# Kernel tuning notes

Hardware: AMD Instinct MI355X
Metric: run time of the kernel (lower is better)

Reference implementation:

```python
import jax, jax.numpy as jnp
import numpy as np

B, S, H, A = 16, 2048, 1024, 8


def setup_inputs() -> dict:
    key = jax.random.key(0)
    k1, k2, k3, k4 = jax.random.split(key, 4)
    token_embeddings = jax.random.normal(k1, (B, S, H), dtype=jnp.float32)
    aspect_embedding = jax.random.normal(k2, (B, A, H), dtype=jnp.float32)
    # Linear(2H -> H): stored as [2H, H] so we can use x @ W (same math as torch W^T)
    W = jax.random.normal(k3, (2 * H, H), dtype=jnp.float32) * (1.0 / np.sqrt(2 * H))
    b = jnp.zeros((H,), dtype=jnp.float32)
    v = jax.random.uniform(k4, (H,), dtype=jnp.float32)  # torch.rand init
    return {"token_embeddings": token_embeddings, "aspect_embedding": aspect_embedding,
            "W": W, "b": b, "v": v}


def reference(token_embeddings, aspect_embedding, W, b, v):
    # mean-pool aspect tokens -> [B, 1, H], broadcast over seq
    asp = jnp.mean(aspect_embedding, axis=1, keepdims=True)
    asp = jnp.broadcast_to(asp, token_embeddings.shape)          # [B, S, H]
    combined = jnp.concatenate([token_embeddings, asp], axis=2)   # [B, S, 2H]
    energy = jnp.tanh(combined @ W + b)                           # [B, S, H]
    scores = jnp.einsum('bsh,h->bs', energy, v)                   # [B, S]
    weights = jax.nn.softmax(scores, axis=1)                      # [B, S]
    # token * weights + token  ==  token * (1 + weights)
    return token_embeddings * (1.0 + weights[:, :, None])
```

## Files before the change

kernel.cpp:

```cpp
#include <hip/hip_runtime.h>
#include <hip/hip_bf16.h>
#include <stdint.h>


#define SEQ 2048
#define H 1024
#define MTOT 32768
#define BK 32

typedef __bf16 bf16x8 __attribute__((ext_vector_type(8)));
typedef float  f32x4  __attribute__((ext_vector_type(4)));

__device__ __forceinline__ void async16(const void* g, void* l) {
  __builtin_amdgcn_global_load_lds(
      (const __attribute__((address_space(1))) unsigned*)g,
      (__attribute__((address_space(3))) unsigned*)l, 16, 0, 0);
}

__device__ __forceinline__ unsigned f2bfraw(float f) {
  unsigned x = __float_as_uint(f);
  return (x + 0x7fffu + ((x >> 16) & 1u)) >> 16;
}
__device__ __forceinline__ float fast_tanh(float x) {
  x = fminf(fmaxf(x, -40.0f), 40.0f);
  float e = __expf(2.0f * x);
  return 1.0f - 2.0f / (e + 1.0f);
}

__global__ __launch_bounds__(256) void convert_tok(
    const float* __restrict__ in, unsigned short* __restrict__ ob) {
  const size_t i = ((size_t)blockIdx.x * 256 + threadIdx.x) * 8;
  const f32x4 a = *reinterpret_cast<const f32x4*>(in + i);
  const f32x4 b = *reinterpret_cast<const f32x4*>(in + i + 4);
  uint4 r;
  r.x = f2bfraw(a[0]) | (f2bfraw(a[1]) << 16);
  r.y = f2bfraw(a[2]) | (f2bfraw(a[3]) << 16);
  r.z = f2bfraw(b[0]) | (f2bfraw(b[1]) << 16);
  r.w = f2bfraw(b[2]) | (f2bfraw(b[3]) << 16);
  *reinterpret_cast<uint4*>(ob + i) = r;
}

__global__ __launch_bounds__(256) void transpose_w(
    const float* __restrict__ W, unsigned short* __restrict__ WT) {
  __shared__ float tile[32][33];
  const int x = threadIdx.x;
  const int y = threadIdx.y;
  const int n0 = blockIdx.x * 32, k0 = blockIdx.y * 32;
#pragma unroll
  for (int i = 0; i < 4; ++i)
    tile[y + 8 * i][x] = W[(size_t)(k0 + y + 8 * i) * H + n0 + x];
  __syncthreads();
#pragma unroll
  for (int i = 0; i < 4; ++i)
    WT[(size_t)(n0 + y + 8 * i) * H + k0 + x] = (unsigned short)f2bfraw(tile[x][y + 8 * i]);
}

__global__ __launch_bounds__(256) void aspect_c(
    const float* __restrict__ asp,
    const float* __restrict__ W,
    const float* __restrict__ bias,
    float* __restrict__ cpart) {
  const int b = blockIdx.x, nc = blockIdx.y, kc = blockIdx.z;
  const int t = threadIdx.x;
  const int lane = t & 63, w = t >> 6;
  __shared__ float am[256];
  __shared__ f32x4 red[4][64];
  {
    const int k = kc * 256 + t;
    float s = 0.f;
#pragma unroll
    for (int a = 0; a < 8; ++a) s += asp[(size_t)(b * 8 + a) * H + k];
    am[t] = s * 0.125f;
  }
  __syncthreads();
  const int n = nc * 256 + lane * 4;
  const float* wp = W + (size_t)(H + kc * 256 + w * 64) * H + n;
  f32x4 acc = {};
#pragma unroll 8
  for (int k = 0; k < 64; ++k) {
    const f32x4 wv = *reinterpret_cast<const f32x4*>(wp + (size_t)k * H);
    const float a = am[w * 64 + k];
    acc[0] += a * wv[0]; acc[1] += a * wv[1];
    acc[2] += a * wv[2]; acc[3] += a * wv[3];
  }
  red[w][lane] = acc;
  __syncthreads();
  if (w == 0) {
    f32x4 r = red[0][lane];
#pragma unroll
    for (int i = 1; i < 4; ++i) {
      const f32x4 x = red[i][lane];
      r[0] += x[0]; r[1] += x[1]; r[2] += x[2]; r[3] += x[3];
    }
    if (kc == 0) {
      r[0] += bias[n];     r[1] += bias[n + 1];
      r[2] += bias[n + 2]; r[3] += bias[n + 3];
    }
    *reinterpret_cast<f32x4*>(cpart + (size_t)kc * 16 * H + b * H + n) = r;
  }
}

__global__ __launch_bounds__(256) void gemm_score(
    const __hip_bfloat16* __restrict__ tokb,
    const __hip_bfloat16* __restrict__ wt,
    const float* __restrict__ cpart,
    const float* __restrict__ v,
    float* __restrict__ part) {
  __shared__ __hip_bfloat16 As[128 * BK];
  __shared__ __hip_bfloat16 Bs[128 * BK];
  const int t = threadIdx.x;
  const int lane = t & 63;
  const int w = t >> 6;
  const int wm = w >> 1, wn = w & 1;
  const unsigned bidl = blockIdx.x + (blockIdx.y << 3);
  const unsigned nb = ((bidl & 7u) << 8) | (bidl >> 3);
  const int bx = nb & 7;
  const int by = nb >> 3;
  const int m0 = by * 128;
  const int n0 = bx * 128;
  const int bb = by >> 4;

  f32x4 acc[4][4] = {};

  const int srow = t >> 2, scol = (t & 3) * 8;
  const __hip_bfloat16* ga = tokb + (size_t)(m0 + srow) * H + scol;
  const __hip_bfloat16* gb = wt + (size_t)(n0 + srow) * H + scol;
  __hip_bfloat16* la0 = As + t * 8;
  __hip_bfloat16* la1 = As + t * 8 + 64 * BK;
  __hip_bfloat16* lb0 = Bs + t * 8;
  __hip_bfloat16* lb1 = Bs + t * 8 + 64 * BK;

  const int quad = lane >> 4, l16 = lane & 15;

  for (int k0 = 0; k0 < H; k0 += BK) {
    __syncthreads();
    async16(ga + k0, la0);
    async16(ga + k0 + (size_t)64 * H, la1);
    async16(gb + k0, lb0);
    async16(gb + k0 + (size_t)64 * H, lb1);
    __syncthreads();

    bf16x8 af[4], bf[4];
#pragma unroll
    for (int mi = 0; mi < 4; ++mi)
      af[mi] = *reinterpret_cast<const bf16x8*>(
          As + (wm * 64 + mi * 16 + l16) * BK + quad * 8);
#pragma unroll
    for (int ni = 0; ni < 4; ++ni)
      bf[ni] = *reinterpret_cast<const bf16x8*>(
          Bs + (wn * 64 + ni * 16 + l16) * BK + quad * 8);
#pragma unroll
    for (int mi = 0; mi < 4; ++mi)
#pragma unroll
      for (int ni = 0; ni < 4; ++ni)
        acc[mi][ni] = __builtin_amdgcn_mfma_f32_16x16x32_bf16(
            af[mi], bf[ni], acc[mi][ni], 0, 0, 0);
  }

  float vv[4], cc[4];
#pragma unroll
  for (int ni = 0; ni < 4; ++ni) {
    const int gn = n0 + wn * 64 + ni * 16 + l16;
    vv[ni] = v[gn];
    float s = cpart[(size_t)bb * H + gn];
    s += cpart[(size_t)1 * 16 * H + bb * H + gn];
    s += cpart[(size_t)2 * 16 * H + bb * H + gn];
    s += cpart[(size_t)3 * 16 * H + bb * H + gn];
    cc[ni] = s;
  }
  const size_t pbase = ((size_t)bx * 2 + wn) * MTOT + m0;
#pragma unroll
  for (int mi = 0; mi < 4; ++mi) {
#pragma unroll
    for (int r = 0; r < 4; ++r) {
      float s = 0.f;
#pragma unroll
      for (int ni = 0; ni < 4; ++ni)
        s += fast_tanh(acc[mi][ni][r] + cc[ni]) * vv[ni];
#pragma unroll
      for (int msk = 1; msk < 16; msk <<= 1) s += __shfl_xor(s, msk, 64);
      if (l16 == 0)
        part[pbase + wm * 64 + mi * 16 + quad * 4 + r] = s;
    }
  }
}

__global__ __launch_bounds__(1024) void softmax_k(
    const float* __restrict__ part, float* __restrict__ wts) {
  const int b = blockIdx.x, t = threadIdx.x;
  const int lane = t & 63, w = t >> 6;
  __shared__ float red[16];
  const int s0 = t * 2;
  float sx = 0.f, sy = 0.f;
#pragma unroll
  for (int p = 0; p < 16; ++p) {
    const float2 x = *reinterpret_cast<const float2*>(
        part + (size_t)p * MTOT + b * SEQ + s0);
    sx += x.x; sy += x.y;
  }
  float m = fmaxf(sx, sy);
#pragma unroll
  for (int o = 1; o < 64; o <<= 1) m = fmaxf(m, __shfl_xor(m, o, 64));
  if (lane == 0) red[w] = m;
  __syncthreads();
  m = red[0];
#pragma unroll
  for (int i = 1; i < 16; ++i) m = fmaxf(m, red[i]);
  __syncthreads();
  const float e0 = __expf(sx - m), e1 = __expf(sy - m);
  float sum = e0 + e1;
#pragma unroll
  for (int o = 1; o < 64; o <<= 1) sum += __shfl_xor(sum, o, 64);
  if (lane == 0) red[w] = sum;
  __syncthreads();
  sum = 0.f;
#pragma unroll
  for (int i = 0; i < 16; ++i) sum += red[i];
  const float inv = 1.0f / sum;
  float2 o2; o2.x = e0 * inv; o2.y = e1 * inv;
  *reinterpret_cast<float2*>(wts + (size_t)b * SEQ + s0) = o2;
}

__global__ __launch_bounds__(256) void scale_k(
    const float* __restrict__ tok, const float* __restrict__ wts,
    float* __restrict__ out) {
  const size_t i = ((size_t)blockIdx.x * 256 + threadIdx.x) * 4;
  const float wm = 1.0f + wts[i >> 10];
  const f32x4 a = *reinterpret_cast<const f32x4*>(tok + i);
  f32x4 o;
  o[0] = a[0] * wm; o[1] = a[1] * wm; o[2] = a[2] * wm; o[3] = a[3] * wm;
  *reinterpret_cast<f32x4*>(out + i) = o;
}

extern "C" void kernel_launch(void* const* d_in, const int* in_sizes, int n_in,
                              void* d_out, int out_size, void* d_ws, size_t ws_size,
                              hipStream_t stream) {
  const float* tok  = (const float*)d_in[0];
  const float* asp  = (const float*)d_in[1];
  const float* W    = (const float*)d_in[2];
  const float* bias = (const float*)d_in[3];
  const float* v    = (const float*)d_in[4];
  float* out = (float*)d_out;

  unsigned short* tokb_u = (unsigned short*)out;
  float*          cpart  = out + 16777216;
  float*          part   = out + 32505856;
  unsigned short* WT_u   = (unsigned short*)(out + 33030144);
  float* wts = (ws_size >= (size_t)(SEQ * 16 * 4)) ? (float*)d_ws
                                                   : (float*)d_in[1];

  convert_tok<<<16384, 256, 0, stream>>>(tok, tokb_u);
  transpose_w<<<dim3(32, 32), dim3(32, 8), 0, stream>>>(W, WT_u);
  aspect_c<<<dim3(16, 4, 4), 256, 0, stream>>>(asp, W, bias, cpart);
  gemm_score<<<dim3(8, 256), 256, 0, stream>>>(
      (const __hip_bfloat16*)tokb_u, (const __hip_bfloat16*)WT_u,
      cpart, v, part);
  softmax_k<<<16, 1024, 0, stream>>>(part, wts);
  scale_k<<<32768, 256, 0, stream>>>(tok, wts, out);
}
```

Measured before the change: 369.2 us.

## Fuse token bf16 conversion into GEMM loads and merge prep kernels

Drops the separate token fp32-to-bf16 conversion pass. The GEMM now loads fp32 token tiles into registers, converts them to bf16 in-kernel, and writes them to LDS, prefetching the next K-slice during compute. The W transpose and aspect projection kernels are merged into one launch. This removes a full write and reread of a 64MB bf16 token copy plus two launches. The cost is that the GEMM reads twice as many A bytes per tile (fp32) and uses synchronous register staging instead of async LDS loads, with up to 8x redundant fp32 reads across the N blocks.

```diff
diff --git a/kernel.cpp b/kernel.cpp
--- a/kernel.cpp
+++ b/kernel.cpp
@@ -21,87 +21,79 @@
   unsigned x = __float_as_uint(f);
   return (x + 0x7fffu + ((x >> 16) & 1u)) >> 16;
 }
+__device__ __forceinline__ unsigned pk2(float x, float y) {
+  return f2bfraw(x) | (f2bfraw(y) << 16);
+}
 __device__ __forceinline__ float fast_tanh(float x) {
   x = fminf(fmaxf(x, -40.0f), 40.0f);
   float e = __expf(2.0f * x);
   return 1.0f - 2.0f / (e + 1.0f);
 }
 
-__global__ __launch_bounds__(256) void convert_tok(
-    const float* __restrict__ in, unsigned short* __restrict__ ob) {
-  const size_t i = ((size_t)blockIdx.x * 256 + threadIdx.x) * 8;
-  const f32x4 a = *reinterpret_cast<const f32x4*>(in + i);
-  const f32x4 b = *reinterpret_cast<const f32x4*>(in + i + 4);
-  uint4 r;
-  r.x = f2bfraw(a[0]) | (f2bfraw(a[1]) << 16);
-  r.y = f2bfraw(a[2]) | (f2bfraw(a[3]) << 16);
-  r.z = f2bfraw(b[0]) | (f2bfraw(b[1]) << 16);
-  r.w = f2bfraw(b[2]) | (f2bfraw(b[3]) << 16);
-  *reinterpret_cast<uint4*>(ob + i) = r;
-}
-
-__global__ __launch_bounds__(256) void transpose_w(
-    const float* __restrict__ W, unsigned short* __restrict__ WT) {
-  __shared__ float tile[32][33];
-  const int x = threadIdx.x;
-  const int y = threadIdx.y;
-  const int n0 = blockIdx.x * 32, k0 = blockIdx.y * 32;
-#pragma unroll
-  for (int i = 0; i < 4; ++i)
-    tile[y + 8 * i][x] = W[(size_t)(k0 + y + 8 * i) * H + n0 + x];
-  __syncthreads();
-#pragma unroll
-  for (int i = 0; i < 4; ++i)
-    WT[(size_t)(n0 + y + 8 * i) * H + k0 + x] = (unsigned short)f2bfraw(tile[x][y + 8 * i]);
-}
-
-__global__ __launch_bounds__(256) void aspect_c(
+__global__ __launch_bounds__(256) void prep_k(
+    const float* __restrict__ W,
     const float* __restrict__ asp,
-    const float* __restrict__ W,
     const float* __restrict__ bias,
+    unsigned short* __restrict__ WT,
     float* __restrict__ cpart) {
-  const int b = blockIdx.x, nc = blockIdx.y, kc = blockIdx.z;
+  __shared__ __align__(16) float shbuf[1312];
   const int t = threadIdx.x;
-  const int lane = t & 63, w = t >> 6;
-  __shared__ float am[256];
-  __shared__ f32x4 red[4][64];
-  {
-    const int k = kc * 256 + t;
-    float s = 0.f;
-#pragma unroll
-    for (int a = 0; a < 8; ++a) s += asp[(size_t)(b * 8 + a) * H + k];
-    am[t] = s * 0.125f;
-  }
-  __syncthreads();
-  const int n = nc * 256 + lane * 4;
-  const float* wp = W + (size_t)(H + kc * 256 + w * 64) * H + n;
-  f32x4 acc = {};
+  if (blockIdx.x < 1024) {
+    float (*tile)[33] = reinterpret_cast<float(*)[33]>(shbuf);
+    const int x = t & 31, y = t >> 5;
+    const int n0 = (blockIdx.x & 31) * 32, k0 = (blockIdx.x >> 5) * 32;
+#pragma unroll
+    for (int i = 0; i < 4; ++i)
+      tile[y + 8 * i][x] = W[(size_t)(k0 + y + 8 * i) * H + n0 + x];
+    __syncthreads();
+#pragma unroll
+    for (int i = 0; i < 4; ++i)
+      WT[(size_t)(n0 + y + 8 * i) * H + k0 + x] =
+          (unsigned short)f2bfraw(tile[x][y + 8 * i]);
+  } else {
+    const int idx = blockIdx.x - 1024;
+    const int b = idx & 15, nc = (idx >> 4) & 3, kc = idx >> 6;
+    const int lane = t & 63, w = t >> 6;
+    float* am = shbuf;
+    f32x4* red = reinterpret_cast<f32x4*>(shbuf + 256);
+    {
+      const int k = kc * 256 + t;
+      float s = 0.f;
+#pragma unroll
+      for (int a = 0; a < 8; ++a) s += asp[(size_t)(b * 8 + a) * H + k];
+      am[t] = s * 0.125f;
+    }
+    __syncthreads();
+    const int n = nc * 256 + lane * 4;
+    const float* wp = W + (size_t)(H + kc * 256 + w * 64) * H + n;
+    f32x4 acc = {};
 #pragma unroll 8
-  for (int k = 0; k < 64; ++k) {
-    const f32x4 wv = *reinterpret_cast<const f32x4*>(wp + (size_t)k * H);
-    const float a = am[w * 64 + k];
-    acc[0] += a * wv[0]; acc[1] += a * wv[1];
-    acc[2] += a * wv[2]; acc[3] += a * wv[3];
-  }
-  red[w][lane] = acc;
-  __syncthreads();
-  if (w == 0) {
-    f32x4 r = red[0][lane];
-#pragma unroll
-    for (int i = 1; i < 4; ++i) {
-      const f32x4 x = red[i][lane];
-      r[0] += x[0]; r[1] += x[1]; r[2] += x[2]; r[3] += x[3];
-    }
-    if (kc == 0) {
-      r[0] += bias[n];     r[1] += bias[n + 1];
-      r[2] += bias[n + 2]; r[3] += bias[n + 3];
-    }
-    *reinterpret_cast<f32x4*>(cpart + (size_t)kc * 16 * H + b * H + n) = r;
+    for (int k = 0; k < 64; ++k) {
+      const f32x4 wv = *reinterpret_cast<const f32x4*>(wp + (size_t)k * H);
+      const float a = am[w * 64 + k];
+      acc[0] += a * wv[0]; acc[1] += a * wv[1];
+      acc[2] += a * wv[2]; acc[3] += a * wv[3];
+    }
+    red[w * 64 + lane] = acc;
+    __syncthreads();
+    if (w == 0) {
+      f32x4 r = red[lane];
+#pragma unroll
+      for (int i = 1; i < 4; ++i) {
+        const f32x4 x = red[i * 64 + lane];
+        r[0] += x[0]; r[1] += x[1]; r[2] += x[2]; r[3] += x[3];
+      }
+      if (kc == 0) {
+        r[0] += bias[n];     r[1] += bias[n + 1];
+        r[2] += bias[n + 2]; r[3] += bias[n + 3];
+      }
+      *reinterpret_cast<f32x4*>(cpart + (size_t)kc * 16 * H + b * H + n) = r;
+    }
   }
 }
 
 __global__ __launch_bounds__(256) void gemm_score(
-    const __hip_bfloat16* __restrict__ tokb,
+    const float* __restrict__ tokf,
     const __hip_bfloat16* __restrict__ wt,
     const float* __restrict__ cpart,
     const float* __restrict__ v,
@@ -123,7 +115,7 @@
   f32x4 acc[4][4] = {};
 
   const int srow = t >> 2, scol = (t & 3) * 8;
-  const __hip_bfloat16* ga = tokb + (size_t)(m0 + srow) * H + scol;
+  const float* ga = tokf + (size_t)(m0 + srow) * H + scol;
   const __hip_bfloat16* gb = wt + (size_t)(n0 + srow) * H + scol;
   __hip_bfloat16* la0 = As + t * 8;
   __hip_bfloat16* la1 = As + t * 8 + 64 * BK;
@@ -132,13 +124,30 @@
 
   const int quad = lane >> 4, l16 = lane & 15;
 
+  f32x4 a0l = *reinterpret_cast<const f32x4*>(ga);
+  f32x4 a0h = *reinterpret_cast<const f32x4*>(ga + 4);
+  f32x4 a1l = *reinterpret_cast<const f32x4*>(ga + (size_t)64 * H);
+  f32x4 a1h = *reinterpret_cast<const f32x4*>(ga + (size_t)64 * H + 4);
+
   for (int k0 = 0; k0 < H; k0 += BK) {
     __syncthreads();
-    async16(ga + k0, la0);
-    async16(ga + k0 + (size_t)64 * H, la1);
     async16(gb + k0, lb0);
     async16(gb + k0 + (size_t)64 * H, lb1);
-    __syncthreads();
+    uint4 r0, r1;
+    r0.x = pk2(a0l[0], a0l[1]); r0.y = pk2(a0l[2], a0l[3]);
+    r0.z = pk2(a0h[0], a0h[1]); r0.w = pk2(a0h[2], a0h[3]);
+    r1.x = pk2(a1l[0], a1l[1]); r1.y = pk2(a1l[2], a1l[3]);
+    r1.z = pk2(a1h[0], a1h[1]); r1.w = pk2(a1h[2], a1h[3]);
+    *reinterpret_cast<uint4*>(la0) = r0;
+    *reinterpret_cast<uint4*>(la1) = r1;
+    __syncthreads();
+
+    if (k0 + BK < H) {
+      a0l = *reinterpret_cast<const f32x4*>(ga + k0 + BK);
+      a0h = *reinterpret_cast<const f32x4*>(ga + k0 + BK + 4);
+      a1l = *reinterpret_cast<const f32x4*>(ga + k0 + BK + (size_t)64 * H);
+      a1h = *reinterpret_cast<const f32x4*>(ga + k0 + BK + (size_t)64 * H + 4);
+    }
 
     bf16x8 af[4], bf[4];
 #pragma unroll
@@ -242,19 +251,15 @@
   const float* v    = (const float*)d_in[4];
   float* out = (float*)d_out;
 
-  unsigned short* tokb_u = (unsigned short*)out;
   float*          cpart  = out + 16777216;
   float*          part   = out + 32505856;
   unsigned short* WT_u   = (unsigned short*)(out + 33030144);
   float* wts = (ws_size >= (size_t)(SEQ * 16 * 4)) ? (float*)d_ws
                                                    : (float*)d_in[1];
 
-  convert_tok<<<16384, 256, 0, stream>>>(tok, tokb_u);
-  transpose_w<<<dim3(32, 32), dim3(32, 8), 0, stream>>>(W, WT_u);
-  aspect_c<<<dim3(16, 4, 4), 256, 0, stream>>>(asp, W, bias, cpart);
-  gemm_score<<<dim3(8, 256), 256, 0, stream>>>(
-      (const __hip_bfloat16*)tokb_u, (const __hip_bfloat16*)WT_u,
-      cpart, v, part);
+  prep_k<<<1280, 256, 0, stream>>>(W, asp, bias, WT_u, cpart);
+  gemm_score<<<dim3(8, 256), 256, 0, stream>>>(tok, (const __hip_bfloat16*)WT_u,
+                                               cpart, v, part);
   softmax_k<<<16, 1024, 0, stream>>>(part, wts);
   scale_k<<<32768, 256, 0, stream>>>(tok, wts, out);
 }
```

New measurement: 380.5 us. 3.0% more time.
